# Performance work log

Hardware: AMD Instinct MI355X
Metric: run time of the kernel (lower is better)

The kernel has to match this reference:

```python
import jax, jax.numpy as jnp
import numpy as np

BN_EPS = 1e-5

def setup_inputs() -> dict:
    key = jax.random.key(0)
    k1, k2 = jax.random.split(key)
    B, C, H, W, K = 256, 2048, 7, 7, 16
    featmap = jax.random.normal(k1, (B, C, H, W), dtype=jnp.float32)
    w16 = jax.random.normal(k2, (K, C), dtype=jnp.float32) * 0.02  # 1x1 conv weight
    bn_gamma = jnp.ones((K,), jnp.float32)
    bn_beta = jnp.zeros((K,), jnp.float32)
    bn_mean = jnp.zeros((K,), jnp.float32)
    bn_var = jnp.ones((K,), jnp.float32)
    return {"featmap": featmap, "w16": w16, "bn_gamma": bn_gamma,
            "bn_beta": bn_beta, "bn_mean": bn_mean, "bn_var": bn_var}

def reference(featmap, w16, bn_gamma, bn_beta, bn_mean, bn_var):
    # featmap: [B, 2048, 7, 7]; 1x1 conv -> featcov16: [B, 16, 7, 7]
    featcov16 = jnp.einsum('bchw,kc->bkhw', featmap, w16)
    # BatchNorm2d(16), inference-style with running stats
    inv = bn_gamma / jnp.sqrt(bn_var + BN_EPS)
    featcov16 = featcov16 * inv[None, :, None, None] + (bn_beta - bn_mean * inv)[None, :, None, None]
    # Loop-free bilinear pooling: original repeats featcov16[:,i] to 2048 ch,
    # multiplies with featmap, and AvgPool2d(7) -> mean over HxW.
    HW = featmap.shape[2] * featmap.shape[3]
    feat_matrix = jnp.einsum('bkhw,bchw->bkc', featcov16, featmap) / HW  # [B,16,2048]
    bp_out_feat = feat_matrix.reshape(feat_matrix.shape[0], -1)  # [B, 32768]
    return bp_out_feat
```

## Files before the change

### kernel.cpp

```cpp
#include <hip/hip_runtime.h>

#define BATCH 256
#define CDIM  2048
#define HW    49
#define KDIM  16
#define CHUNK 512
#define TILE  128
#define ROWP  52

__global__ __launch_bounds__(256) void pconv_kernel(
    const float* __restrict__ fm, const float* __restrict__ w16,
    float* __restrict__ Ppart)
{
    __shared__ __align__(16) float fm_t[TILE * ROWP + 16];
    __shared__ __align__(16) float w_t[TILE * KDIM];

    const int tid = threadIdx.x;
    const int b   = blockIdx.x >> 2;
    const int q   = blockIdx.x & 3;
    const int c0  = q * CHUNK;
    const int h4  = tid & 15;
    const int cs  = tid >> 4;

    float acc[KDIM][4];
    #pragma unroll
    for (int k = 0; k < KDIM; ++k) {
        acc[k][0] = 0.f; acc[k][1] = 0.f; acc[k][2] = 0.f; acc[k][3] = 0.f;
    }

    const float* fmb = fm + (size_t)b * CDIM * HW;

    for (int tile = 0; tile < CHUNK / TILE; ++tile) {
        const int ct = c0 + tile * TILE;
        __syncthreads();
        const float4* src = (const float4*)(fmb + ct * HW);
        for (int i = tid; i < (TILE * HW) / 4; i += 256) {
            float4 v = src[i];
            int e = i * 4;
            int cl = e / HW; int h = e - cl * HW; fm_t[cl * ROWP + h] = v.x;
            e++; cl = e / HW; h = e - cl * HW;    fm_t[cl * ROWP + h] = v.y;
            e++; cl = e / HW; h = e - cl * HW;    fm_t[cl * ROWP + h] = v.z;
            e++; cl = e / HW; h = e - cl * HW;    fm_t[cl * ROWP + h] = v.w;
        }
        for (int i = tid; i < KDIM * TILE; i += 256) {
            int kk = i >> 7; int cc = i & 127;
            w_t[cc * KDIM + kk] = w16[kk * CDIM + ct + cc];
        }
        __syncthreads();
        #pragma unroll 2
        for (int j = 0; j < 8; ++j) {
            const int cc = cs * 8 + j;
            float4 f = *(const float4*)&fm_t[cc * ROWP + 4 * h4];
            const float4* wq = (const float4*)&w_t[cc * KDIM];
            float wv[16];
            *(float4*)&wv[0]  = wq[0];
            *(float4*)&wv[4]  = wq[1];
            *(float4*)&wv[8]  = wq[2];
            *(float4*)&wv[12] = wq[3];
            #pragma unroll
            for (int k = 0; k < 16; ++k) {
                acc[k][0] += wv[k] * f.x;
                acc[k][1] += wv[k] * f.y;
                acc[k][2] += wv[k] * f.z;
                acc[k][3] += wv[k] * f.w;
            }
        }
    }

    __syncthreads();
    float* red = fm_t;
    for (int r = 0; r < 4; ++r) {
        #pragma unroll
        for (int kk = 0; kk < 4; ++kk)
            #pragma unroll
            for (int hl = 0; hl < 4; ++hl)
                red[cs * 272 + h4 * 17 + kk * 4 + hl] = acc[r * 4 + kk][hl];
        __syncthreads();
        const int kp = r * 4 + (tid >> 6);
        const int hw = tid & 63;
        if (hw < HW) {
            float s = 0.f;
            const int base = (hw >> 2) * 17 + (tid >> 6) * 4 + (hw & 3);
            #pragma unroll
            for (int c = 0; c < 16; ++c) s += red[c * 272 + base];
            Ppart[(size_t)blockIdx.x * 784 + kp * HW + hw] = s;
        }
        __syncthreads();
    }
}

__global__ __launch_bounds__(256) void bp_kernel(
    const float* __restrict__ fm, const float* __restrict__ Ppart,
    const float* __restrict__ gamma, const float* __restrict__ beta,
    const float* __restrict__ mean, const float* __restrict__ var,
    float* __restrict__ out)
{
    __shared__ __align__(16) float Pt[HW * KDIM];
    __shared__ __align__(16) float fm_s[256 * HW];

    const int tid = threadIdx.x;
    const int b   = blockIdx.x >> 3;
    const int c0  = (blockIdx.x & 7) * 256;

    for (int p = tid; p < 784; p += 256) {
        const float* pp = Ppart + (size_t)(b * 4) * 784 + p;
        float s = pp[0] + pp[784] + pp[1568] + pp[2352];
        int kk = p / HW; int hw = p - kk * HW;
        float inv   = gamma[kk] * rsqrtf(var[kk] + 1e-5f);
        float shift = beta[kk] - mean[kk] * inv;
        Pt[hw * KDIM + kk] = (s * inv + shift) * (1.0f / 49.0f);
    }

    {
        const float4* src = (const float4*)(fm + ((size_t)b * CDIM + c0) * HW);
        float4* dst = (float4*)fm_s;
        #pragma unroll 7
        for (int i = tid; i < (256 * HW) / 4; i += 256) dst[i] = src[i];
    }
    __syncthreads();

    float acc[16];
    #pragma unroll
    for (int i = 0; i < 16; ++i) acc[i] = 0.f;

    const float* row = fm_s + tid * HW;
    #pragma unroll 7
    for (int hw = 0; hw < HW; ++hw) {
        float f = row[hw];
        const float4* pv = (const float4*)&Pt[hw * KDIM];
        float4 p0 = pv[0], p1 = pv[1], p2 = pv[2], p3 = pv[3];
        acc[0]  += p0.x * f; acc[1]  += p0.y * f; acc[2]  += p0.z * f; acc[3]  += p0.w * f;
        acc[4]  += p1.x * f; acc[5]  += p1.y * f; acc[6]  += p1.z * f; acc[7]  += p1.w * f;
        acc[8]  += p2.x * f; acc[9]  += p2.y * f; acc[10] += p2.z * f; acc[11] += p2.w * f;
        acc[12] += p3.x * f; acc[13] += p3.y * f; acc[14] += p3.z * f; acc[15] += p3.w * f;
    }

    float* ob = out + (size_t)b * (KDIM * CDIM) + c0 + tid;
    #pragma unroll
    for (int kk = 0; kk < 16; ++kk) ob[kk * CDIM] = acc[kk];
}

extern "C" void kernel_launch(void* const* d_in, const int* in_sizes, int n_in,
                              void* d_out, int out_size, void* d_ws, size_t ws_size,
                              hipStream_t stream) {
    const float* fm    = (const float*)d_in[0];
    const float* w16   = (const float*)d_in[1];
    const float* gamma = (const float*)d_in[2];
    const float* beta  = (const float*)d_in[3];
    const float* mean  = (const float*)d_in[4];
    const float* var   = (const float*)d_in[5];
    float* out   = (float*)d_out;
    float* Ppart = (float*)d_ws;

    pconv_kernel<<<BATCH * 4, 256, 0, stream>>>(fm, w16, Ppart);
    bp_kernel<<<BATCH * 8, 256, 0, stream>>>(fm, Ppart, gamma, beta, mean, var, out);
}
```

Measured before the change: 215.2 us.

## Restructure conv stage as per-wave hw mapping and add separate BN reduce kernel

The 1x1-conv kernel now copies featmap tiles straight into shared memory without transposing or padding, and maps each lane to one spatial position. Each wave handles 32 channels and reads the weights as wave-uniform float4 loads from global memory instead of staging them in shared memory. The partial-result layout changes to hw-major with k innermost, and a new small kernel sums the four channel-chunk partials and applies BatchNorm and the 1/49 scale. The pooling kernel then reads those scaled results directly from global/L2 as uniform loads, dropping its own reduction and shared staging. This adds a third launch and scalar/global loads inside the inner loops, and leaves 15 of 64 lanes idle per wave in the conv stage.

```diff
diff --git a/kernel.cpp b/kernel.cpp
--- a/kernel.cpp
+++ b/kernel.cpp
@@ -6,118 +6,105 @@
 #define KDIM  16
 #define CHUNK 512
 #define TILE  128
-#define ROWP  52
 
 __global__ __launch_bounds__(256) void pconv_kernel(
     const float* __restrict__ fm, const float* __restrict__ w16,
     float* __restrict__ Ppart)
 {
-    __shared__ __align__(16) float fm_t[TILE * ROWP + 16];
-    __shared__ __align__(16) float w_t[TILE * KDIM];
+    __shared__ __align__(16) float fm_t[6304];
 
     const int tid = threadIdx.x;
     const int b   = blockIdx.x >> 2;
     const int q   = blockIdx.x & 3;
-    const int c0  = q * CHUNK;
-    const int h4  = tid & 15;
-    const int cs  = tid >> 4;
+    const int hw  = tid & 63;
+    const int wv  = __builtin_amdgcn_readfirstlane(tid >> 6);
 
-    float acc[KDIM][4];
+    float acc[16];
     #pragma unroll
-    for (int k = 0; k < KDIM; ++k) {
-        acc[k][0] = 0.f; acc[k][1] = 0.f; acc[k][2] = 0.f; acc[k][3] = 0.f;
-    }
+    for (int k = 0; k < 16; ++k) acc[k] = 0.f;
 
     const float* fmb = fm + (size_t)b * CDIM * HW;
 
-    for (int tile = 0; tile < CHUNK / TILE; ++tile) {
-        const int ct = c0 + tile * TILE;
+    for (int tile = 0; tile < 4; ++tile) {
+        const int ct = q * CHUNK + tile * TILE;
         __syncthreads();
         const float4* src = (const float4*)(fmb + ct * HW);
-        for (int i = tid; i < (TILE * HW) / 4; i += 256) {
-            float4 v = src[i];
-            int e = i * 4;
-            int cl = e / HW; int h = e - cl * HW; fm_t[cl * ROWP + h] = v.x;
-            e++; cl = e / HW; h = e - cl * HW;    fm_t[cl * ROWP + h] = v.y;
-            e++; cl = e / HW; h = e - cl * HW;    fm_t[cl * ROWP + h] = v.z;
-            e++; cl = e / HW; h = e - cl * HW;    fm_t[cl * ROWP + h] = v.w;
-        }
-        for (int i = tid; i < KDIM * TILE; i += 256) {
-            int kk = i >> 7; int cc = i & 127;
-            w_t[cc * KDIM + kk] = w16[kk * CDIM + ct + cc];
-        }
+        float4* dst = (float4*)fm_t;
+        #pragma unroll
+        for (int it = 0; it < 6; ++it) dst[it * 256 + tid] = src[it * 256 + tid];
+        if (tid < 32) dst[1536 + tid] = src[1536 + tid];
         __syncthreads();
+
+        const float* wbase = w16 + ct + wv * 32;
         #pragma unroll 2
-        for (int j = 0; j < 8; ++j) {
-            const int cc = cs * 8 + j;
-            float4 f = *(const float4*)&fm_t[cc * ROWP + 4 * h4];
-            const float4* wq = (const float4*)&w_t[cc * KDIM];
-            float wv[16];
-            *(float4*)&wv[0]  = wq[0];
-            *(float4*)&wv[4]  = wq[1];
-            *(float4*)&wv[8]  = wq[2];
-            *(float4*)&wv[12] = wq[3];
+        for (int j4 = 0; j4 < 8; ++j4) {
+            const int cc = wv * 32 + j4 * 4;
+            float f0 = fm_t[(cc + 0) * HW + hw];
+            float f1 = fm_t[(cc + 1) * HW + hw];
+            float f2 = fm_t[(cc + 2) * HW + hw];
+            float f3 = fm_t[(cc + 3) * HW + hw];
             #pragma unroll
             for (int k = 0; k < 16; ++k) {
-                acc[k][0] += wv[k] * f.x;
-                acc[k][1] += wv[k] * f.y;
-                acc[k][2] += wv[k] * f.z;
-                acc[k][3] += wv[k] * f.w;
+                const float4 wq = *(const float4*)(wbase + k * CDIM + j4 * 4);
+                acc[k] += wq.x * f0 + wq.y * f1 + wq.z * f2 + wq.w * f3;
             }
         }
     }
 
     __syncthreads();
     float* red = fm_t;
-    for (int r = 0; r < 4; ++r) {
+    #pragma unroll
+    for (int k = 0; k < 16; ++k) red[wv * 1088 + hw * 17 + k] = acc[k];
+    __syncthreads();
+
+    const int e = tid * 4;
+    if (e < 784) {
+        float4 o;
         #pragma unroll
-        for (int kk = 0; kk < 4; ++kk)
-            #pragma unroll
-            for (int hl = 0; hl < 4; ++hl)
-                red[cs * 272 + h4 * 17 + kk * 4 + hl] = acc[r * 4 + kk][hl];
-        __syncthreads();
-        const int kp = r * 4 + (tid >> 6);
-        const int hw = tid & 63;
-        if (hw < HW) {
-            float s = 0.f;
-            const int base = (hw >> 2) * 17 + (tid >> 6) * 4 + (hw & 3);
-            #pragma unroll
-            for (int c = 0; c < 16; ++c) s += red[c * 272 + base];
-            Ppart[(size_t)blockIdx.x * 784 + kp * HW + hw] = s;
+        for (int j = 0; j < 4; ++j) {
+            const int ee = e + j, hh = ee >> 4, kk = ee & 15;
+            ((float*)&o)[j] = red[hh * 17 + kk] + red[1088 + hh * 17 + kk]
+                            + red[2176 + hh * 17 + kk] + red[3264 + hh * 17 + kk];
         }
-        __syncthreads();
+        *(float4*)(Ppart + (size_t)blockIdx.x * 784 + e) = o;
+    }
+}
+
+__global__ __launch_bounds__(256) void preduce_kernel(
+    const float* __restrict__ Ppart,
+    const float* __restrict__ gamma, const float* __restrict__ beta,
+    const float* __restrict__ mean, const float* __restrict__ var,
+    float* __restrict__ Pbn)
+{
+    const int b = blockIdx.x;
+    const float* pp = Ppart + (size_t)b * 4 * 784;
+    for (int p = threadIdx.x; p < 784; p += 256) {
+        float s = pp[p] + pp[p + 784] + pp[p + 1568] + pp[p + 2352];
+        const int kk = p & 15;
+        float inv   = gamma[kk] * rsqrtf(var[kk] + 1e-5f);
+        float shift = beta[kk] - mean[kk] * inv;
+        Pbn[(size_t)b * 784 + p] = (s * inv + shift) * (1.0f / 49.0f);
     }
 }
 
 __global__ __launch_bounds__(256) void bp_kernel(
-    const float* __restrict__ fm, const float* __restrict__ Ppart,
-    const float* __restrict__ gamma, const float* __restrict__ beta,
-    const float* __restrict__ mean, const float* __restrict__ var,
+    const float* __restrict__ fm, const float* __restrict__ Pbn,
     float* __restrict__ out)
 {
-    __shared__ __align__(16) float Pt[HW * KDIM];
     __shared__ __align__(16) float fm_s[256 * HW];
 
     const int tid = threadIdx.x;
     const int b   = blockIdx.x >> 3;
     const int c0  = (blockIdx.x & 7) * 256;
 
-    for (int p = tid; p < 784; p += 256) {
-        const float* pp = Ppart + (size_t)(b * 4) * 784 + p;
-        float s = pp[0] + pp[784] + pp[1568] + pp[2352];
-        int kk = p / HW; int hw = p - kk * HW;
-        float inv   = gamma[kk] * rsqrtf(var[kk] + 1e-5f);
-        float shift = beta[kk] - mean[kk] * inv;
-        Pt[hw * KDIM + kk] = (s * inv + shift) * (1.0f / 49.0f);
-    }
+    const float4* src = (const float4*)(fm + ((size_t)b * CDIM + c0) * HW);
+    float4* dst = (float4*)fm_s;
+    #pragma unroll
+    for (int i = 0; i < 12; ++i) dst[i * 256 + tid] = src[i * 256 + tid];
+    if (tid < 64) dst[3072 + tid] = src[3072 + tid];
+    __syncthreads();
 
-    {
-        const float4* src = (const float4*)(fm + ((size_t)b * CDIM + c0) * HW);
-        float4* dst = (float4*)fm_s;
-        #pragma unroll 7
-        for (int i = tid; i < (256 * HW) / 4; i += 256) dst[i] = src[i];
-    }
-    __syncthreads();
+    const float* Pb = Pbn + (size_t)b * 784;
 
     float acc[16];
     #pragma unroll
@@ -127,8 +114,10 @@
     #pragma unroll 7
     for (int hw = 0; hw < HW; ++hw) {
         float f = row[hw];
-        const float4* pv = (const float4*)&Pt[hw * KDIM];
-        float4 p0 = pv[0], p1 = pv[1], p2 = pv[2], p3 = pv[3];
+        const float4 p0 = *(const float4*)(Pb + hw * 16 + 0);
+        const float4 p1 = *(const float4*)(Pb + hw * 16 + 4);
+        const float4 p2 = *(const float4*)(Pb + hw * 16 + 8);
+        const float4 p3 = *(const float4*)(Pb + hw * 16 + 12);
         acc[0]  += p0.x * f; acc[1]  += p0.y * f; acc[2]  += p0.z * f; acc[3]  += p0.w * f;
         acc[4]  += p1.x * f; acc[5]  += p1.y * f; acc[6]  += p1.z * f; acc[7]  += p1.w * f;
         acc[8]  += p2.x * f; acc[9]  += p2.y * f; acc[10] += p2.z * f; acc[11] += p2.w * f;
@@ -151,7 +140,9 @@
     const float* var   = (const float*)d_in[5];
     float* out   = (float*)d_out;
     float* Ppart = (float*)d_ws;
+    float* Pbn   = Ppart + (size_t)1024 * 784;
 
     pconv_kernel<<<BATCH * 4, 256, 0, stream>>>(fm, w16, Ppart);
-    bp_kernel<<<BATCH * 8, 256, 0, stream>>>(fm, Ppart, gamma, beta, mean, var, out);
+    preduce_kernel<<<BATCH, 256, 0, stream>>>(Ppart, gamma, beta, mean, var, Pbn);
+    bp_kernel<<<BATCH * 8, 256, 0, stream>>>(fm, Pbn, out);
 }
```

New measurement: 219.8 us. +2.1%, slower.
